# Kernel tuning notes

Measured on AMD Instinct MI355X. Metric: run time of the kernel, lower is better.

The kernel has to match this reference:

```python
import jax, jax.numpy as jnp
import numpy as np

N_NET = 4000000   # length of concatenated model output values
R = 1000000       # number of rotated sp blocks (s0=9, s1=3)
NG = 1024         # number of geometries in the single bsize group
B = 64            # basis size (orbitals per molecule)
NE = 7            # number of elements for Eref
EREP = 2000000    # repulsive pair terms
ROT_LEN = 2 + R * 9


def setup_inputs() -> dict:
    key = jax.random.key(0)
    ks = jax.random.split(key, 14)
    net_vals = jax.random.normal(ks[0], (N_NET,), jnp.float32)
    rot_tensors = jax.random.normal(ks[1], (R, 9, 3), jnp.float32)
    S = jax.random.normal(ks[2], (NG, B, B), jnp.float32)
    S = 0.5 * (S + jnp.swapaxes(S, -2, -1))  # overlap is symmetric
    G = jax.random.normal(ks[3], (NG, B, B), jnp.float32)
    G = 0.5 * (G + jnp.swapaxes(G, -2, -1))  # gamma matrix is symmetric
    rho = jax.random.normal(ks[4], (NG, B, B), jnp.float32)
    qneutral = jax.random.uniform(ks[5], (NG, B, 1), dtype=jnp.float32)
    occ_rho_mask = (jax.random.uniform(ks[6], (NG, B, B)) > 0.5).astype(jnp.float32)
    phiS = 0.1 * jax.random.normal(ks[7], (NG, B, B), jnp.float32)
    zcounts = jax.random.uniform(ks[8], (1, NE), dtype=jnp.float32)
    ref_vars = jax.random.normal(ks[9], (NE,), jnp.float32)
    gather_rot = jax.random.randint(ks[10], (R * 3,), 0, N_NET)
    gather_oper = jax.random.randint(ks[11], (NG * B * B,), 0, ROT_LEN)
    gather_rep = jax.random.randint(ks[12], (EREP,), 0, N_NET)
    segsum_rep = jnp.sort(jax.random.randint(ks[13], (EREP,), 0, NG))
    return dict(net_vals=net_vals, rot_tensors=rot_tensors, S=S, G=G, rho=rho,
                qneutral=qneutral, occ_rho_mask=occ_rho_mask, phiS=phiS,
                zcounts=zcounts, ref_vars=ref_vars, gather_rot=gather_rot,
                gather_oper=gather_oper, gather_rep=gather_rep, segsum_rep=segsum_rep)


def reference(net_vals, rot_tensors, S, G, rho, qneutral, occ_rho_mask, phiS,
              zcounts, ref_vars, gather_rot, gather_oper, gather_rep, segsum_rep):
    ng, b, _ = S.shape
    # --- rotation stage: gather net_vals, batched small matmul [R,9,3]@[R,3,1]
    rot_vals = net_vals[gather_rot].reshape(-1, 3)[:, :, None]          # [R,3,1]
    rot = jnp.matmul(rot_tensors, rot_vals)[:, :, 0]                    # [R,9]
    rot_out = jnp.concatenate([jnp.array([0.0, 1.0], S.dtype), rot.reshape(-1)])
    # --- operator gather: build H blocks per geometry
    H = rot_out[gather_oper].reshape(ng, b, b)
    # --- charge fluctuations and coulomb matrix
    qbasis = rho * S
    dQ = qneutral - jnp.sum(qbasis, axis=2, keepdims=True)              # [ng,b,1]
    ep = jnp.matmul(G, dQ)                                              # [ng,b,1]
    couMat = -0.5 * S * (ep + jnp.swapaxes(ep, -2, -1))
    F = H + couMat
    # --- repulsive energy: gather + segment-sum over geometries
    Erep = jax.ops.segment_sum(net_vals[gather_rep], segsum_rep, num_segments=ng)
    # --- generalized eigenproblem via provided phiS (S^{-1/2})
    fockp = jnp.swapaxes(phiS, -2, -1) @ (F @ phiS)
    eorb, C = jnp.linalg.eigh(fockp)
    orb = phiS @ C
    orb_filled = occ_rho_mask * orb
    rho_out = 2.0 * (orb_filled @ jnp.swapaxes(orb_filled, -2, -1))
    # --- electronic energy
    ener1 = jnp.sum(rho_out * H, axis=(1, 2))
    ener2 = 0.5 * jnp.squeeze(jnp.swapaxes(dQ, -2, -1) @ (G @ dQ), axis=(1, 2))
    Eelec = ener1 + ener2
    Eref = jnp.dot(zcounts[0], ref_vars)
    return (H, dQ, Erep, eorb, rho_out, Eelec, Eref)
```

## Files before the change

kernel.cpp:

```cpp
#include <hip/hip_runtime.h>

typedef unsigned int uint_t;

#define NGc     1024
#define Bc      64
#define LDA     67
#define LDV     68
#define Rc      1000000
#define NNETc   4000000
#define EREPc   2000000
#define ROTLENc 9000002

#define OFF_H     0
#define OFF_DQ    4194304
#define OFF_EREP  4259840
#define OFF_EORB  4260864
#define OFF_RHO   4326400
#define OFF_EELEC 8520704
#define OFF_EREF  8521728

__global__ void k_rot(const float* __restrict__ rot_t,
                      const int*   __restrict__ gather_rot,
                      const float* __restrict__ net_vals,
                      float*       __restrict__ ws)
{
    int r = blockIdx.x * 256 + threadIdx.x;
    if (r >= Rc) return;
    const int* gr = gather_rot + (size_t)r * 3;
    int i0 = gr[0], i1 = gr[1], i2 = gr[2];
    i0 = ((unsigned)i0 < (unsigned)NNETc) ? i0 : 0;
    i1 = ((unsigned)i1 < (unsigned)NNETc) ? i1 : 0;
    i2 = ((unsigned)i2 < (unsigned)NNETc) ? i2 : 0;
    float v0 = net_vals[i0], v1 = net_vals[i1], v2 = net_vals[i2];
    const float* tt = rot_t + (size_t)r * 27;
    float* wp = ws + (size_t)r * 9;
    #pragma unroll
    for (int c = 0; c < 9; c++)
        wp[c] = tt[c*3+0] * v0 + tt[c*3+1] * v1 + tt[c*3+2] * v2;
}

__global__ void k_hgather4(const int*   __restrict__ idx,
                           const float* __restrict__ ws,
                           float*       __restrict__ out)
{
    int t4 = blockIdx.x * 256 + threadIdx.x;
    const int4 id4 = ((const int4*)idx)[t4];
    float4 hv;
    {
        int id = id4.x;
        hv.x = (id >= 2 && id < ROTLENc) ? ws[id - 2] : ((id == 1) ? 1.0f : 0.0f);
    }
    {
        int id = id4.y;
        hv.y = (id >= 2 && id < ROTLENc) ? ws[id - 2] : ((id == 1) ? 1.0f : 0.0f);
    }
    {
        int id = id4.z;
        hv.z = (id >= 2 && id < ROTLENc) ? ws[id - 2] : ((id == 1) ? 1.0f : 0.0f);
    }
    {
        int id = id4.w;
        hv.w = (id >= 2 && id < ROTLENc) ? ws[id - 2] : ((id == 1) ? 1.0f : 0.0f);
    }
    ((float4*)(out + OFF_H))[t4] = hv;
}

__global__ void k_hgather(const int*   __restrict__ idx,
                          const float* __restrict__ rot_t,
                          const int*   __restrict__ gather_rot,
                          const float* __restrict__ net_vals,
                          float*       __restrict__ out)
{
    int t = blockIdx.x * 256 + threadIdx.x;
    if (t >= NGc * Bc * Bc) return;
    int id = idx[t];
    float hv;
    if (id >= 2 && id < ROTLENc) {
        int k = id - 2;
        int r = k / 9;
        int c = k - r * 9;
        const float* tt = rot_t + (size_t)r * 27 + (size_t)c * 3;
        const int*   gr = gather_rot + (size_t)r * 3;
        int i0 = gr[0], i1 = gr[1], i2 = gr[2];
        i0 = ((unsigned)i0 < (unsigned)NNETc) ? i0 : 0;
        i1 = ((unsigned)i1 < (unsigned)NNETc) ? i1 : 0;
        i2 = ((unsigned)i2 < (unsigned)NNETc) ? i2 : 0;
        hv = tt[0] * net_vals[i0] + tt[1] * net_vals[i1] + tt[2] * net_vals[i2];
    } else {
        hv = (id == 1) ? 1.0f : 0.0f;
    }
    out[OFF_H + t] = hv;
}

__global__ void k_erep_seg(const float* __restrict__ net_vals,
                           const int*   __restrict__ gather_rep,
                           const int*   __restrict__ segsum,
                           const float* __restrict__ zcounts,
                           const float* __restrict__ ref_vars,
                           float*       __restrict__ out)
{
    __shared__ int   sB[2];
    __shared__ float red[256];
    const int g = blockIdx.x, tid = threadIdx.x;

    if (tid < 2) {
        int target = g + tid;
        int lo = 0, hi = EREPc;
        while (lo < hi) {
            int mid = (lo + hi) >> 1;
            if (segsum[mid] < target) lo = mid + 1; else hi = mid;
        }
        sB[tid] = lo;
    }
    __syncthreads();
    const int s = sB[0], e = sB[1];
    float acc = 0.f;
    for (int i = s + tid; i < e; i += 256) {
        int gi = gather_rep[i];
        gi = ((unsigned)gi < (unsigned)NNETc) ? gi : 0;
        acc += net_vals[gi];
    }
    red[tid] = acc;
    __syncthreads();
    for (int sN = 128; sN > 0; sN >>= 1) {
        if (tid < sN) red[tid] += red[tid + sN];
        __syncthreads();
    }
    if (tid == 0) out[OFF_EREP + g] = red[0];

    if (g == 0 && tid == 0) {
        float er = 0.f;
        for (int j = 0; j < 7; j++) er += zcounts[j] * ref_vars[j];
        out[OFF_EREF] = er;
    }
}

__global__ __launch_bounds__(256, 4) void k_geom(
    const float* __restrict__ Sg_,  const float* __restrict__ Gg_,
    const float* __restrict__ rho_, const float* __restrict__ qn_,
    const float* __restrict__ mask_,const float* __restrict__ phiS_,
    float* out)
{
    __shared__ float Ab[Bc * LDA];
    __shared__ float Vb[Bc * LDV];
    __shared__ float dqs[Bc];
    __shared__ float epv[Bc];
    __shared__ float red[256];
    __shared__ float diagA[Bc];
    __shared__ int   perm[Bc];
    __shared__ float2 csCS[32];
    __shared__ float sOffArr[4];

    const int g    = blockIdx.x;
    const int tid  = threadIdx.x;
    const size_t gb = (size_t)g * 4096;

    const float* Sp = Sg_  + gb;
    const float* Gp = Gg_  + gb;
    const float* Rp = rho_ + gb;
    const float* Mp = mask_+ gb;
    const float* Pp = phiS_+ gb;
    const float4* P4 = (const float4*)Pp;
    const float* Hp = out + OFF_H + gb;

    #pragma unroll
    for (int m = 0; m < 16; m++) {
        int e = tid + m * 256;
        int i = e >> 6, j = e & 63;
        Vb[i*LDV + j] = Sp[e];
    }
    __syncthreads();

    {
        int i = tid >> 2, qr = tid & 3;
        float acc = 0.f;
        #pragma unroll
        for (int jj = 0; jj < 16; jj++) {
            int j = qr * 16 + jj;
            acc += Rp[i * 64 + j] * Vb[i*LDV + j];
        }
        acc += __shfl_xor(acc, 1, 64);
        acc += __shfl_xor(acc, 2, 64);
        if (qr == 0) dqs[i] = qn_[(size_t)g * 64 + i] - acc;
    }
    #pragma unroll
    for (int m = 0; m < 16; m++) {
        int e = tid + m * 256;
        int i = e >> 6, j = e & 63;
        Ab[i*LDA + j] = Gp[e];
    }
    __syncthreads();
    {
        int i = tid >> 2, qr = tid & 3;
        float acc = 0.f;
        #pragma unroll
        for (int jj = 0; jj < 16; jj++) {
            int j = qr * 16 + jj;
            acc += Ab[i*LDA + j] * dqs[j];
        }
        acc += __shfl_xor(acc, 1, 64);
        acc += __shfl_xor(acc, 2, 64);
        if (qr == 0) epv[i] = acc;
    }
    __syncthreads();
    float ener2r = 0.f;
    if (tid < 64) {
        float v = dqs[tid] * epv[tid];
        #pragma unroll
        for (int o = 1; o < 64; o <<= 1) v += __shfl_xor(v, o, 64);
        if (tid == 0) ener2r = 0.5f * v;
    }
    #pragma unroll
    for (int m = 0; m < 16; m++) {
        int e = tid + m * 256;
        int i = e >> 6, j = e & 63;
        Ab[i*LDA + j] = Hp[e] - 0.5f * Vb[i*LDV + j] * (epv[i] + epv[j]);
    }
    __syncthreads();

    const int tx = tid & 15, ty = tid >> 4;
    const int row0 = ty * 4, col0 = tx * 4;
    float acc4[4][4];

    #pragma unroll
    for (int u = 0; u < 4; u++)
        #pragma unroll
        for (int v = 0; v < 4; v++) acc4[u][v] = 0.f;
    for (int k = 0; k < 64; k++) {
        float av[4];
        #pragma unroll
        for (int u = 0; u < 4; u++) av[u] = Ab[(row0 + u) * LDA + k];
        union { float4 v4; float f[4]; } b4;
        b4.v4 = P4[k * 16 + tx];
        #pragma unroll
        for (int u = 0; u < 4; u++)
            #pragma unroll
            for (int v = 0; v < 4; v++) acc4[u][v] += av[u] * b4.f[v];
    }
    #pragma unroll
    for (int u = 0; u < 4; u++)
        #pragma unroll
        for (int v = 0; v < 4; v++) Vb[(row0 + u) * LDV + col0 + v] = acc4[u][v];
    __syncthreads();

    #pragma unroll
    for (int u = 0; u < 4; u++)
        #pragma unroll
        for (int v = 0; v < 4; v++) acc4[u][v] = 0.f;
    for (int k = 0; k < 64; k++) {
        union { float4 v4; float f[4]; } a4;
        a4.v4 = P4[k * 16 + ty];
        float bv[4];
        #pragma unroll
        for (int v = 0; v < 4; v++) bv[v] = Vb[k * LDV + col0 + v];
        #pragma unroll
        for (int u = 0; u < 4; u++)
            #pragma unroll
            for (int v = 0; v < 4; v++) acc4[u][v] += a4.f[u] * bv[v];
    }
    {
        float fr = 0.f;
        #pragma unroll
        for (int u = 0; u < 4; u++)
            #pragma unroll
            for (int v = 0; v < 4; v++) {
                Ab[(row0 + u) * LDA + col0 + v] = acc4[u][v];
                fr += acc4[u][v] * acc4[u][v];
            }
        if (tx == ty) {
            #pragma unroll
            for (int u = 0; u < 4; u++) diagA[row0 + u] = acc4[u][u];
        }
        red[tid] = fr;
    }
    __syncthreads();
    for (int sN = 128; sN > 0; sN >>= 1) {
        if (tid < sN) red[tid] += red[tid + sN];
        __syncthreads();
    }
    const float anorm2 = red[0];

    #pragma unroll
    for (int m = 0; m < 17; m++) {
        int e = tid + m * 256;
        if (e < Bc * LDV) Vb[e] = 0.f;
    }
    __syncthreads();
    if (tid < 64) { Vb[tid * LDV + tid] = 1.f; perm[tid] = tid; }

    const float skip2 = anorm2 * 1e-18f;
    const float conv2 = anorm2 * 4e-14f;

    const int myi = tid & 31;
    const int jb  = tid >> 5;
    const int cb  = jb << 3;

    int myP = (myi == 0) ? 63 : myi;
    int myQ = (myi == 0) ? 0  : 63 - myi;
    int iPv = myP * LDV, iQv = myQ * LDV;

    int bi1, bj1, bi2 = 0, bj2 = 1;
    {
        int m = tid, i = 0;
        while (m >= 31 - i) { m -= 31 - i; ++i; }
        bi1 = i; bj1 = i + 1 + m;
    }
    const bool hasB2 = (tid + 256) < 496;
    if (hasB2) {
        int m = tid + 256, i = 0;
        while (m >= 31 - i) { m -= 31 - i; ++i; }
        bi2 = i; bj2 = i + 1 + m;
    }
    int pI1 = (bi1 == 0) ? 63 : bi1, qI1 = (bi1 == 0) ? 0 : 63 - bi1;
    int pJ1 = bj1,                   qJ1 = 63 - bj1;
    int pI2 = (bi2 == 0) ? 63 : bi2, qI2 = (bi2 == 0) ? 0 : 63 - bi2;
    int pJ2 = bj2,                   qJ2 = 63 - bj2;

    #define ADVI(v) v = ((v) == 62) ? 0 : (((v) == 63) ? 63 : (v) + 1)

    for (int sweep = 0; sweep < 10; ++sweep) {
        float offacc = 0.f;
        for (int r = 0; r < 63; r++) {
            if (tid < 32) {
                float app = diagA[myP];
                float aqq = diagA[myQ];
                int mn = min(myP, myQ), mx = max(myP, myQ);
                int apqA = mn * LDA + mx;
                float apq = Ab[apqA];
                float a2 = apq * apq;
                offacc += a2;
                float c = 1.f, s = 0.f;
                if (a2 > skip2) {
                    float tau = (aqq - app) * __builtin_amdgcn_rcpf(apq + apq);
                    float tt = __builtin_amdgcn_rcpf(
                        fabsf(tau) + __builtin_amdgcn_sqrtf(1.f + tau * tau));
                    tt = (tau < 0.f) ? -tt : tt;
                    c = __builtin_amdgcn_rsqf(1.f + tt * tt);
                    s = tt * c;
                    diagA[myP] = app - tt * apq;
                    diagA[myQ] = aqq + tt * apq;
                    Ab[apqA] = 0.f;
                }
                csCS[myi] = make_float2(c, s);
            }
            __syncthreads();

            {
                float2 AI = csCS[bi1], AJ = csCS[bj1];
                if (AI.y != 0.f || AJ.y != 0.f) {
                    int mn, mx;
                    mn = min(pI1,pJ1); mx = max(pI1,pJ1); int aA = mn*LDA + mx;
                    mn = min(pI1,qJ1); mx = max(pI1,qJ1); int aB = mn*LDA + mx;
                    mn = min(qI1,pJ1); mx = max(qI1,pJ1); int aD = mn*LDA + mx;
                    mn = min(qI1,qJ1); mx = max(qI1,qJ1); int aE = mn*LDA + mx;
                    float a = Ab[aA], b = Ab[aB], d = Ab[aD], e = Ab[aE];
                    float a1 = AJ.x*a - AJ.y*b, b1 = AJ.y*a + AJ.x*b;
                    float d1 = AJ.x*d - AJ.y*e, e1 = AJ.y*d + AJ.x*e;
                    Ab[aA] = AI.x*a1 - AI.y*d1;
                    Ab[aD] = AI.y*a1 + AI.x*d1;
                    Ab[aB] = AI.x*b1 - AI.y*e1;
                    Ab[aE] = AI.y*b1 + AI.x*e1;
                }
            }
            if (hasB2) {
                float2 AI = csCS[bi2], AJ = csCS[bj2];
                if (AI.y != 0.f || AJ.y != 0.f) {
                    int mn, mx;
                    mn = min(pI2,pJ2); mx = max(pI2,pJ2); int aA = mn*LDA + mx;
                    mn = min(pI2,qJ2); mx = max(pI2,qJ2); int aB = mn*LDA + mx;
                    mn = min(qI2,pJ2); mx = max(qI2,pJ2); int aD = mn*LDA + mx;
                    mn = min(qI2,qJ2); mx = max(qI2,qJ2); int aE = mn*LDA + mx;
                    float a = Ab[aA], b = Ab[aB], d = Ab[aD], e = Ab[aE];
                    float a1 = AJ.x*a - AJ.y*b, b1 = AJ.y*a + AJ.x*b;
                    float d1 = AJ.x*d - AJ.y*e, e1 = AJ.y*d + AJ.x*e;
                    Ab[aA] = AI.x*a1 - AI.y*d1;
                    Ab[aD] = AI.y*a1 + AI.x*d1;
                    Ab[aB] = AI.x*b1 - AI.y*e1;
                    Ab[aE] = AI.y*b1 + AI.x*e1;
                }
            }
            {
                float2 me = csCS[myi];
                if (me.y != 0.f) {
                    const float cO = me.x, sO = me.y;
                    float4* vp = (float4*)&Vb[iPv + cb];
                    float4* vq = (float4*)&Vb[iQv + cb];
                    #pragma unroll
                    for (int e2 = 0; e2 < 2; e2++) {
                        float4 xp = vp[e2], xq = vq[e2];
                        float4 np, nq;
                        np.x = cO*xp.x - sO*xq.x;  nq.x = sO*xp.x + cO*xq.x;
                        np.y = cO*xp.y - sO*xq.y;  nq.y = sO*xp.y + cO*xq.y;
                        np.z = cO*xp.z - sO*xq.z;  nq.z = sO*xp.z + cO*xq.z;
                        np.w = cO*xp.w - sO*xq.w;  nq.w = sO*xp.w + cO*xq.w;
                        vp[e2] = np; vq[e2] = nq;
                    }
                }
            }
            iPv = (myP == 62) ? 0 : ((myP == 63) ? iPv : iPv + LDV);
            iQv = (myQ == 62) ? 0 : iQv + LDV;
            ADVI(myP); ADVI(myQ);
            ADVI(pI1); ADVI(qI1); ADVI(pJ1); ADVI(qJ1);
            ADVI(pI2); ADVI(qI2); ADVI(pJ2); ADVI(qJ2);
            __syncthreads();
        }
        float t2 = offacc;
        #pragma unroll
        for (int o = 1; o < 32; o <<= 1) t2 += __shfl_xor(t2, o, 64);
        if (tid == 0) sOffArr[0] = t2;
        __syncthreads();
        if (sOffArr[0] < conv2) break;
    }
    #undef ADVI

    if (tid < 64) {
        float e = diagA[tid]; int rk = 0;
        for (int j = 0; j < 64; j++) {
            float ej = diagA[j];
            rk += (ej < e || (ej == e && j < tid)) ? 1 : 0;
        }
        rk &= 63;
        perm[rk] = tid;
        out[OFF_EORB + (size_t)g * 64 + rk] = e;
    }
    __syncthreads();

    {
        int pc0 = perm[col0 + 0] & 63, pc1 = perm[col0 + 1] & 63;
        int pc2 = perm[col0 + 2] & 63, pc3 = perm[col0 + 3] & 63;
        #pragma unroll
        for (int u = 0; u < 4; u++)
            #pragma unroll
            for (int v = 0; v < 4; v++) acc4[u][v] = 0.f;
        for (int kk = 0; kk < 16; kk++) {
            union { float4 v4; float f[4]; } a0, a1, a2u, a3;
            a0.v4  = P4[(row0 + 0) * 16 + kk];
            a1.v4  = P4[(row0 + 1) * 16 + kk];
            a2u.v4 = P4[(row0 + 2) * 16 + kk];
            a3.v4  = P4[(row0 + 3) * 16 + kk];
            #pragma unroll
            for (int t = 0; t < 4; t++) {
                int k = (kk << 2) + t;
                float b0 = Vb[pc0*LDV + k], b1 = Vb[pc1*LDV + k];
                float b2 = Vb[pc2*LDV + k], b3 = Vb[pc3*LDV + k];
                acc4[0][0] += a0.f[t]  * b0; acc4[0][1] += a0.f[t]  * b1;
                acc4[0][2] += a0.f[t]  * b2; acc4[0][3] += a0.f[t]  * b3;
                acc4[1][0] += a1.f[t]  * b0; acc4[1][1] += a1.f[t]  * b1;
                acc4[1][2] += a1.f[t]  * b2; acc4[1][3] += a1.f[t]  * b3;
                acc4[2][0] += a2u.f[t] * b0; acc4[2][1] += a2u.f[t] * b1;
                acc4[2][2] += a2u.f[t] * b2; acc4[2][3] += a2u.f[t] * b3;
                acc4[3][0] += a3.f[t]  * b0; acc4[3][1] += a3.f[t]  * b1;
                acc4[3][2] += a3.f[t]  * b2; acc4[3][3] += a3.f[t]  * b3;
            }
        }
        __syncthreads();
        #pragma unroll
        for (int u = 0; u < 4; u++)
            #pragma unroll
            for (int v = 0; v < 4; v++) Ab[(row0 + u) * LDA + col0 + v] = acc4[u][v];
    }
    __syncthreads();
    #pragma unroll
    for (int m = 0; m < 16; m++) {
        int e = tid + m * 256;
        int i = e >> 6, j = e & 63;
        Ab[i*LDA + j] *= Mp[e];
    }
    __syncthreads();

    #pragma unroll
    for (int u = 0; u < 4; u++)
        #pragma unroll
        for (int v = 0; v < 4; v++) acc4[u][v] = 0.f;
    for (int k = 0; k < 64; k++) {
        float av[4], bv[4];
        #pragma unroll
        for (int u = 0; u < 4; u++) av[u] = Ab[(row0 + u) * LDA + k];
        #pragma unroll
        for (int v = 0; v < 4; v++) bv[v] = Ab[(col0 + v) * LDA + k];
        #pragma unroll
        for (int u = 0; u < 4; u++)
            #pragma unroll
            for (int v = 0; v < 4; v++) acc4[u][v] += av[u] * bv[v];
    }
    {
        float e1 = 0.f;
        float* outR = out + OFF_RHO + gb;
        #pragma unroll
        for (int u = 0; u < 4; u++)
            #pragma unroll
            for (int v = 0; v < 4; v++) {
                float rv = 2.f * acc4[u][v];
                int i = row0 + u, j = col0 + v;
                outR[i * 64 + j] = rv;
                e1 += rv * Hp[i * 64 + j];
            }
        red[tid] = e1;
    }
    __syncthreads();
    for (int sN = 128; sN > 0; sN >>= 1) {
        if (tid < sN) red[tid] += red[tid + sN];
        __syncthreads();
    }
    if (tid == 0) out[OFF_EELEC + g] = red[0] + ener2r;
    if (tid < 64) out[OFF_DQ + (size_t)g * 64 + tid] = dqs[tid];
}

extern "C" void kernel_launch(void* const* d_in, const int* in_sizes, int n_in,
                              void* d_out, int out_size, void* d_ws, size_t ws_size,
                              hipStream_t stream)
{
    (void)in_sizes; (void)n_in; (void)out_size;
    const float* net_vals    = (const float*)d_in[0];
    const float* rot_tensors = (const float*)d_in[1];
    const float* S           = (const float*)d_in[2];
    const float* G           = (const float*)d_in[3];
    const float* rho         = (const float*)d_in[4];
    const float* qneutral    = (const float*)d_in[5];
    const float* mask        = (const float*)d_in[6];
    const float* phiS        = (const float*)d_in[7];
    const float* zcounts     = (const float*)d_in[8];
    const float* ref_vars    = (const float*)d_in[9];
    const int* gather_rot    = (const int*)d_in[10];
    const int* gather_oper   = (const int*)d_in[11];
    const int* gather_rep    = (const int*)d_in[12];
    const int* segsum_rep    = (const int*)d_in[13];

    float* out = (float*)d_out;

    const size_t need = (size_t)Rc * 9 * sizeof(float);
    if (d_ws && ws_size >= need) {
        k_rot<<<(Rc + 255) / 256, 256, 0, stream>>>(rot_tensors, gather_rot,
                                                    net_vals, (float*)d_ws);
        k_hgather4<<<4096, 256, 0, stream>>>(gather_oper, (const float*)d_ws, out);
    } else {
        k_hgather<<<16384, 256, 0, stream>>>(gather_oper, rot_tensors, gather_rot,
                                             net_vals, out);
    }
    k_erep_seg<<<NGc, 256, 0, stream>>>(net_vals, gather_rep, segsum_rep,
                                        zcounts, ref_vars, out);
    k_geom<<<NGc, 256, 0, stream>>>(S, G, rho, qneutral, mask, phiS, out);
}
```

Before: 1.289 ms.

## Fuse H gather and repulsive segment-sum into geometry kernel

```diff
diff --git a/kernel.cpp b/kernel.cpp
--- a/kernel.cpp
+++ b/kernel.cpp
@@ -37,32 +37,6 @@
     #pragma unroll
     for (int c = 0; c < 9; c++)
         wp[c] = tt[c*3+0] * v0 + tt[c*3+1] * v1 + tt[c*3+2] * v2;
-}
-
-__global__ void k_hgather4(const int*   __restrict__ idx,
-                           const float* __restrict__ ws,
-                           float*       __restrict__ out)
-{
-    int t4 = blockIdx.x * 256 + threadIdx.x;
-    const int4 id4 = ((const int4*)idx)[t4];
-    float4 hv;
-    {
-        int id = id4.x;
-        hv.x = (id >= 2 && id < ROTLENc) ? ws[id - 2] : ((id == 1) ? 1.0f : 0.0f);
-    }
-    {
-        int id = id4.y;
-        hv.y = (id >= 2 && id < ROTLENc) ? ws[id - 2] : ((id == 1) ? 1.0f : 0.0f);
-    }
-    {
-        int id = id4.z;
-        hv.z = (id >= 2 && id < ROTLENc) ? ws[id - 2] : ((id == 1) ? 1.0f : 0.0f);
-    }
-    {
-        int id = id4.w;
-        hv.w = (id >= 2 && id < ROTLENc) ? ws[id - 2] : ((id == 1) ? 1.0f : 0.0f);
-    }
-    ((float4*)(out + OFF_H))[t4] = hv;
 }
 
 __global__ void k_hgather(const int*   __restrict__ idx,
@@ -135,10 +109,15 @@
     }
 }
 
+template<int FUSED>
 __global__ __launch_bounds__(256, 4) void k_geom(
     const float* __restrict__ Sg_,  const float* __restrict__ Gg_,
     const float* __restrict__ rho_, const float* __restrict__ qn_,
     const float* __restrict__ mask_,const float* __restrict__ phiS_,
+    const int*   __restrict__ idx_, const float* __restrict__ ws_,
+    const float* __restrict__ net_vals_,
+    const int*   __restrict__ grep_,const int* __restrict__ segsum_,
+    const float* __restrict__ zcounts_, const float* __restrict__ ref_vars_,
     float* out)
 {
     __shared__ float Ab[Bc * LDA];
@@ -150,6 +129,7 @@
     __shared__ int   perm[Bc];
     __shared__ float2 csCS[32];
     __shared__ float sOffArr[4];
+    __shared__ int   sB[2];
 
     const int g    = blockIdx.x;
     const int tid  = threadIdx.x;
@@ -161,7 +141,24 @@
     const float* Mp = mask_+ gb;
     const float* Pp = phiS_+ gb;
     const float4* P4 = (const float4*)Pp;
-    const float* Hp = out + OFF_H + gb;
+    float* outH = out + OFF_H + gb;
+
+    if (FUSED) {
+        if (tid < 2) {
+            int target = g + tid;
+            int lo = 0, hi = EREPc;
+            while (lo < hi) {
+                int mid = (lo + hi) >> 1;
+                if (segsum_[mid] < target) lo = mid + 1; else hi = mid;
+            }
+            sB[tid] = lo;
+        }
+        if (g == 0 && tid == 255) {
+            float er = 0.f;
+            for (int j = 0; j < 7; j++) er += zcounts_[j] * ref_vars_[j];
+            out[OFF_EREF] = er;
+        }
+    }
 
     #pragma unroll
     for (int m = 0; m < 16; m++) {
@@ -183,6 +180,15 @@
         acc += __shfl_xor(acc, 2, 64);
         if (qr == 0) dqs[i] = qn_[(size_t)g * 64 + i] - acc;
     }
+    float racc = 0.f;
+    if (FUSED) {
+        const int s = sB[0], e = sB[1];
+        for (int i = s + tid; i < e; i += 256) {
+            int gi = grep_[i];
+            gi = ((unsigned)gi < (unsigned)NNETc) ? gi : 0;
+            racc += net_vals_[gi];
+        }
+    }
     #pragma unroll
     for (int m = 0; m < 16; m++) {
         int e = tid + m * 256;
@@ -214,7 +220,16 @@
     for (int m = 0; m < 16; m++) {
         int e = tid + m * 256;
         int i = e >> 6, j = e & 63;
-        Ab[i*LDA + j] = Hp[e] - 0.5f * Vb[i*LDV + j] * (epv[i] + epv[j]);
+        float hv;
+        if (FUSED) {
+            int id = idx_[gb + e];
+            hv = (id >= 2 && id < ROTLENc) ? ws_[id - 2]
+                                           : ((id == 1) ? 1.0f : 0.0f);
+            outH[e] = hv;
+        } else {
+            hv = outH[e];
+        }
+        Ab[i*LDA + j] = hv - 0.5f * Vb[i*LDV + j] * (epv[i] + epv[j]);
     }
     __syncthreads();
 
@@ -493,7 +508,7 @@
                 float rv = 2.f * acc4[u][v];
                 int i = row0 + u, j = col0 + v;
                 outR[i * 64 + j] = rv;
-                e1 += rv * Hp[i * 64 + j];
+                e1 += rv * outH[i * 64 + j];
             }
         red[tid] = e1;
     }
@@ -504,6 +519,15 @@
     }
     if (tid == 0) out[OFF_EELEC + g] = red[0] + ener2r;
     if (tid < 64) out[OFF_DQ + (size_t)g * 64 + tid] = dqs[tid];
+
+    if (FUSED) {
+        #pragma unroll
+        for (int o = 1; o < 64; o <<= 1) racc += __shfl_xor(racc, o, 64);
+        if ((tid & 63) == 0) sOffArr[tid >> 6] = racc;
+        __syncthreads();
+        if (tid == 0)
+            out[OFF_EREP + g] = sOffArr[0] + sOffArr[1] + sOffArr[2] + sOffArr[3];
+    }
 }
 
 extern "C" void kernel_launch(void* const* d_in, const int* in_sizes, int n_in,
@@ -532,12 +556,18 @@
     if (d_ws && ws_size >= need) {
         k_rot<<<(Rc + 255) / 256, 256, 0, stream>>>(rot_tensors, gather_rot,
                                                     net_vals, (float*)d_ws);
-        k_hgather4<<<4096, 256, 0, stream>>>(gather_oper, (const float*)d_ws, out);
+        k_geom<1><<<NGc, 256, 0, stream>>>(S, G, rho, qneutral, mask, phiS,
+                                           gather_oper, (const float*)d_ws,
+                                           net_vals, gather_rep, segsum_rep,
+                                           zcounts, ref_vars, out);
     } else {
         k_hgather<<<16384, 256, 0, stream>>>(gather_oper, rot_tensors, gather_rot,
                                              net_vals, out);
-    }
-    k_erep_seg<<<NGc, 256, 0, stream>>>(net_vals, gather_rep, segsum_rep,
-                                        zcounts, ref_vars, out);
-    k_geom<<<NGc, 256, 0, stream>>>(S, G, rho, qneutral, mask, phiS, out);
+        k_erep_seg<<<NGc, 256, 0, stream>>>(net_vals, gather_rep, segsum_rep,
+                                            zcounts, ref_vars, out);
+        k_geom<0><<<NGc, 256, 0, stream>>>(S, G, rho, qneutral, mask, phiS,
+                                           nullptr, nullptr, nullptr,
+                                           nullptr, nullptr, nullptr, nullptr,
+                                           out);
+    }
 }
```

After: 1.270 ms. Within noise of the previous version (-1.5%).
